# Kernel tuning notes

Hardware: AMD Instinct MI355X
Metric: run time of the kernel (lower is better)

Reference implementation:

```python
import jax, jax.numpy as jnp
import numpy as np


def conv1x1(x, w, b):
    # x: [B,C,H,W], w: [O,C], b: [O]
    return jnp.einsum('bchw,oc->bohw', x, w) + b[None, :, None, None]


def conv2d_same(x, w, b):
    # x: [B,C,H,W], w: [O,I,kh,kw]
    y = jax.lax.conv_general_dilated(x, w, (1, 1), 'SAME',
                                     dimension_numbers=('NCHW', 'OIHW', 'NCHW'))
    return y + b[None, :, None, None]


def l2norm_c(x):
    # F.normalize(x, dim=1): x / max(||x||_2, eps)
    n = jnp.sqrt(jnp.sum(x * x, axis=1, keepdims=True))
    return x / jnp.maximum(n, 1e-12)


def warp_volume(k, disps, directs):
    # Plane-sweep warp. grid_sample(bilinear, border, align_corners=True) with a
    # pure horizontal shift: y-coords equal the identity grid exactly, so
    # bilinear interpolation reduces to 1-D interpolation along W.
    # k: [B,C,H,W], disps: [D], directs: [B,1,1,1] -> [B,C,H,W,D]
    B, C, H, W = k.shape
    dt = k.dtype
    base = jnp.arange(W, dtype=dt)                                   # pixel x
    # normalized shift disp*2 maps to disp*(W-1) pixels (align_corners=True)
    shift = disps.astype(dt)[None, :, None] * directs.reshape(B, 1, 1) * (W - 1)
    px = jnp.clip(base[None, None, :] + shift, 0.0, W - 1)            # [B,D,W] (border pad)
    x0 = jnp.floor(px).astype(jnp.int32)
    x1 = jnp.minimum(x0 + 1, W - 1)
    f = (px - x0.astype(dt))[:, None, None, :, :]                     # [B,1,1,D,W]
    gather = jax.vmap(lambda xb, ib: xb[:, :, ib])                    # [B,C,H,D,W]
    g0 = gather(k, x0)
    g1 = gather(k, x1)
    wk = g0 * (1.0 - f) + g1 * f                                      # [B,C,H,D,W]
    return jnp.transpose(wk, (0, 1, 2, 4, 3))                         # [B,C,H,W,D]


def setup_inputs() -> dict:
    key = jax.random.key(0)
    ks = jax.random.split(key, 16)
    B, C, H, W = 4, 128, 96, 320
    Cm, D = C // 4, 32
    f32 = jnp.float32
    inp = {
        't_feat': jax.random.normal(ks[0], (B, C, H, W), f32),
        's_feat': jax.random.normal(ks[1], (B, C, H, W), f32),
        'directs': jnp.ones((B, 1, 1, 1), f32),
        'image_shape': 320,
        'disps': jnp.arange(D, dtype=f32) * 0.01,
        'wq': jax.random.normal(ks[2], (Cm, C), f32) * 0.05,
        'bq': jnp.zeros((Cm,), f32),
        'wkc': jax.random.normal(ks[3], (Cm, C), f32) * 0.05,
        'bkc': jnp.zeros((Cm,), f32),
        'metric': jnp.eye(Cm, dtype=f32),
        'alpha': jnp.asarray(10.0, f32),
        'beta': jnp.asarray(0.0, f32),
        'w_cf': jax.random.normal(ks[4], (1, 1, 3, 3), f32) * 0.1,
        'b_cf': jnp.zeros((1,), f32),
        'w_da': jax.random.normal(ks[5], (D, 2 * Cm), f32) * 0.05,
        'b_da': jnp.zeros((D,), f32),
        'w_ex': jax.random.normal(ks[6], (C, D), f32) * 0.05,
        'b_ex': jnp.zeros((C,), f32),
        'w_fg': jax.random.normal(ks[7], (1, 2 * C), f32) * 0.05,
        'b_fg': jnp.zeros((1,), f32),
        'w_rd': jax.random.normal(ks[8], (C, C, 3, 3), f32) * 0.02,
        'b_rd': jnp.zeros((C,), f32),
        'w_se1': jax.random.normal(ks[9], (C // 16, C), f32) * 0.1,
        'w_se2': jax.random.normal(ks[10], (C, C // 16), f32) * 0.1,
    }
    return inp


def reference(t_feat, s_feat, directs, image_shape, disps,
              wq, bq, wkc, bkc, metric, alpha, beta,
              w_cf, b_cf, w_da, b_da, w_ex, b_ex, w_fg, b_fg,
              w_rd, b_rd, w_se1, w_se2):
    del image_shape  # only used when train_image_size is set (it is None here)
    q = l2norm_c(conv1x1(t_feat, wq, bq))          # [B,Cm,H,W]
    k = l2norm_c(conv1x1(s_feat, wkc, bkc))        # [B,Cm,H,W]
    warped = warp_volume(k, disps, directs)        # [B,Cm,H,W,D]
    M = 0.5 * (metric + metric.T)
    q_proj = jnp.einsum('bchw,cd->bdhw', q, M)
    sim = jnp.einsum('bdhw,bdhwk->bhwk', q_proj, warped)
    sim = jnp.tanh(alpha * sim + beta)             # [B,H,W,D]
    Cv = jnp.transpose(sim, (0, 3, 1, 2))          # [B,D,H,W]
    B, D, H, W = Cv.shape
    # Conv3d(1,1,(1,3,3)) == per-slice 2D 3x3 conv
    Cf = conv2d_same(Cv.reshape(B * D, 1, H, W), w_cf, b_cf).reshape(B, D, H, W)
    k_mean = warped.mean(axis=-1)                  # [B,Cm,H,W]
    da = jax.nn.sigmoid(conv1x1(jnp.concatenate([q, k_mean], axis=1), w_da, b_da))
    Cf = Cf * da
    P = jax.nn.softmax(Cf, axis=1)                 # [B,D,H,W]
    cost_feat = conv1x1(P, w_ex, b_ex)             # [B,C,H,W]
    g = jax.nn.sigmoid(conv1x1(jnp.concatenate([t_feat, cost_feat], axis=1), w_fg, b_fg))
    fused = g * t_feat + (1.0 - g) * cost_feat
    x = conv2d_same(fused, w_rd, b_rd)
    # SELayer(reduction=16)
    y = x.mean(axis=(2, 3))                        # [B,C]
    y = jax.nn.relu(y @ w_se1.T)
    y = jax.nn.sigmoid(y @ w_se2.T)
    x = x * y[:, :, None, None]
    x = jax.nn.elu(x)
    return (x, P)
```

## Files before the change

### kernel.cpp

```cpp
#include <hip/hip_runtime.h>
#include <hip/hip_bf16.h>
#include <math.h>


typedef __hip_bfloat16 bf16;
typedef unsigned short u16;
typedef __attribute__((ext_vector_type(8))) __bf16 bf16x8;
typedef __attribute__((ext_vector_type(4))) float f4;

#define DEVI static __device__ __forceinline__
DEVI float bf2f(bf16 x) { return __bfloat162float(x); }
DEVI bf16  f2bf(float x) { return __float2bfloat16(x); }
DEVI u16 bfbits(float x) { bf16 h = f2bf(x); return *(u16*)&h; }
DEVI float sigmoidf_(float x) { return 1.0f / (1.0f + expf(-x)); }

constexpr int B_ = 4, C_ = 128, H_ = 96, W_ = 320, CM = 32, D_ = 32;
constexpr int HW = H_ * W_;
constexpr int QPLANE = CM * HW;
constexpr int XN = B_ * C_ * HW;
constexpr int PLN = B_ * D_ * HW;

__device__ __align__(16) float g_scratch[8 * PLN];
__device__ __align__(16) u16   g_fused[XN];
__device__ __align__(16) u16   g_wt[9 * 128 * 128];
__device__ float g_ysum[512];
__device__ float g_se[512];
__device__ int   g_flag[1];

DEVI float ldin(const void* p, int i, int isb) {
    float v;
    if (isb) v = bf2f(((const bf16*)p)[i]);
    else     v = ((const float*)p)[i];
    return v;
}
DEVI void stout(void* p, int i, float v, int isb) {
    if (isb) ((bf16*)p)[i] = f2bf(v);
    else     ((float*)p)[i] = v;
}

__global__ __launch_bounds__(256) void k_detect(
    const void* __restrict__ t, const void* __restrict__ wqp)
{
    __shared__ int bad;
    int tid = threadIdx.x;
    if (tid == 0) bad = 0;
    __syncthreads();
    int mybad = 0;
    for (int i = tid; i < 4096; i += 256) {
        float v = bf2f(((const bf16*)t)[i]);
        if (!(v == v) || fabsf(v) > 64.0f) mybad = 1;
        float u = bf2f(((const bf16*)wqp)[i]);
        if (!(u == u) || fabsf(u) > 64.0f) mybad = 1;
    }
    if (mybad) atomicOr(&bad, 1);
    g_ysum[tid] = 0.f;
    g_ysum[tid + 256] = 0.f;
    __syncthreads();
    if (tid == 0) g_flag[0] = bad ? 0 : 1;
}

__global__ __launch_bounds__(256) void k_wprep(
    const void* __restrict__ w_rd, u16* __restrict__ gw)
{
    int isb = g_flag[0];
    int i = blockIdx.x * 256 + threadIdx.x;
    if (i >= 9 * 128 * 128) return;
    int pos = i >> 14, rem = i & 16383, co = rem >> 7, ci = rem & 127;
    gw[i] = bfbits(ldin(w_rd, (co * 128 + ci) * 9 + pos, isb));
}

__global__ __launch_bounds__(320) void k_qk(
    const void* __restrict__ t_feat, const void* __restrict__ s_feat,
    const void* __restrict__ wq, const void* __restrict__ bq,
    const void* __restrict__ wkc, const void* __restrict__ bkc,
    float* __restrict__ qout, float* __restrict__ kout)
{
    __shared__ float WST[C_ * CM];
    __shared__ float BS[CM];
    int isb = g_flag[0];
    int h = blockIdx.x, b = blockIdx.y, which = blockIdx.z;
    const void* in = which ? s_feat : t_feat;
    const void* wm = which ? wkc : wq;
    const void* bb = which ? bkc : bq;
    float* out = which ? kout : qout;
    int tid = threadIdx.x;
    for (int i = tid; i < C_ * CM; i += 320) {
        int o = i >> 7, c = i & 127;
        WST[c * CM + o] = ldin(wm, i, isb);
    }
    if (tid < CM) BS[tid] = ldin(bb, tid, isb);
    __syncthreads();
    int w = tid;
    float acc[CM];
    #pragma unroll
    for (int o = 0; o < CM; o++) acc[o] = BS[o];
    int base = (b * C_) * HW + h * W_ + w;
    for (int c = 0; c < C_; c++) {
        float v = ldin(in, base + c * HW, isb);
        #pragma unroll
        for (int o = 0; o < CM; o++) acc[o] += v * WST[c * CM + o];
    }
    float n = 0.f;
    #pragma unroll
    for (int o = 0; o < CM; o++) n += acc[o] * acc[o];
    float s = 1.0f / fmaxf(sqrtf(n), 1e-12f);
    float* op = out + (b * CM) * HW + h * W_ + w;
    #pragma unroll
    for (int o = 0; o < CM; o++) op[o * HW] = acc[o] * s;
}

__global__ __launch_bounds__(320, 3) void k_cost(
    const float* __restrict__ qbuf, const float* __restrict__ kbuf,
    const void* __restrict__ metric, const void* __restrict__ disps,
    const void* __restrict__ directs, const void* __restrict__ alpha_p,
    const void* __restrict__ beta_p, const void* __restrict__ w_da,
    const void* __restrict__ b_da,
    float* __restrict__ Cv, float* __restrict__ da)
{
    __shared__ float KS[CM][W_];
    __shared__ float MS[CM][CM];
    __shared__ float WDA[D_ * 64];
    __shared__ float BDA[D_];
    __shared__ float SH[D_];
    int isb = g_flag[0];
    int h = blockIdx.x, b = blockIdx.y, tid = threadIdx.x, w = tid;
    for (int i = tid; i < CM * CM; i += 320) {
        int c = i >> 5, d = i & 31;
        MS[c][d] = 0.5f * (ldin(metric, c * CM + d, isb) + ldin(metric, d * CM + c, isb));
    }
    for (int i = tid; i < D_ * 64; i += 320) WDA[i] = ldin(w_da, i, isb);
    if (tid < D_) {
        BDA[tid] = ldin(b_da, tid, isb);
        SH[tid] = ldin(disps, tid, isb) * ldin(directs, b, isb) * (float)(W_ - 1);
    }
    const float* kp = kbuf + b * QPLANE + h * W_;
    for (int c = 0; c < CM; c++) KS[c][w] = kp[c * HW + w];
    __syncthreads();

    float qp[CM], dqa[CM];
    #pragma unroll
    for (int d = 0; d < CM; d++) { qp[d] = 0.f; dqa[d] = 0.f; }
    const float* qpp = qbuf + b * QPLANE + h * W_ + w;
    for (int c = 0; c < CM; c++) {
        float v = qpp[c * HW];
        #pragma unroll
        for (int d = 0; d < CM; d++) qp[d] += v * MS[c][d];
        #pragma unroll
        for (int d = 0; d < D_; d++) dqa[d] += v * WDA[d * 64 + c];
    }

    float km[CM];
    #pragma unroll
    for (int c = 0; c < CM; c++) km[c] = 0.f;
    float alpha = ldin(alpha_p, 0, isb), beta = ldin(beta_p, 0, isb);
    float* cvp = Cv + (b * D_) * HW + h * W_ + w;
    for (int d = 0; d < D_; d++) {
        float px = fminf(fmaxf((float)w + SH[d], 0.f), (float)(W_ - 1));
        int x0 = (int)floorf(px);
        int x1 = min(x0 + 1, W_ - 1);
        float f = px - (float)x0;
        float sim = 0.f;
        #pragma unroll
        for (int c = 0; c < CM; c++) {
            float g0 = KS[c][x0], g1 = KS[c][x1];
            float val = g0 * (1.0f - f) + g1 * f;
            sim += qp[c] * val;
            km[c] += val;
        }
        cvp[d * HW] = tanhf(alpha * sim + beta);
    }

    #pragma unroll
    for (int c = 0; c < CM; c++) km[c] *= (1.0f / (float)D_);
    float* dap = da + (b * D_) * HW + h * W_ + w;
    for (int d = 0; d < D_; d++) {
        float s = BDA[d] + dqa[d];
        #pragma unroll
        for (int c = 0; c < CM; c++) s += WDA[d * 64 + 32 + c] * km[c];
        dap[d * HW] = sigmoidf_(s);
    }
}

__global__ __launch_bounds__(320) void k_cf_softmax(
    const float* __restrict__ Cv, const float* __restrict__ da,
    const void* __restrict__ w_cf, const void* __restrict__ b_cf,
    float* __restrict__ Pf, void* __restrict__ dout)
{
    __shared__ float R[3][322];
    int isb = g_flag[0];
    int h = blockIdx.x, b = blockIdx.y, tid = threadIdx.x, w = tid;
    float wcf[9];
    #pragma unroll
    for (int i = 0; i < 9; i++) wcf[i] = ldin(w_cf, i, isb);
    float bcf = ldin(b_cf, 0, isb);
    float vals[D_];
    for (int d = 0; d < D_; d++) {
        const float* base = Cv + ((b * D_ + d) * H_) * W_;
        #pragma unroll
        for (int r = 0; r < 3; r++) {
            int hh = h + r - 1;
            R[r][w + 1] = (hh >= 0 && hh < H_) ? base[hh * W_ + w] : 0.f;
        }
        if (tid == 0) {
            R[0][0] = R[1][0] = R[2][0] = 0.f;
            R[0][321] = R[1][321] = R[2][321] = 0.f;
        }
        __syncthreads();
        float s = bcf;
        #pragma unroll
        for (int r = 0; r < 3; r++)
            #pragma unroll
            for (int kw = 0; kw < 3; kw++)
                s += R[r][w + kw] * wcf[r * 3 + kw];
        vals[d] = s * da[((b * D_ + d) * H_ + h) * W_ + w];
        __syncthreads();
    }
    float m = vals[0];
    #pragma unroll
    for (int d = 1; d < D_; d++) m = fmaxf(m, vals[d]);
    float sum = 0.f;
    #pragma unroll
    for (int d = 0; d < D_; d++) { vals[d] = expf(vals[d] - m); sum += vals[d]; }
    float inv = 1.0f / sum;
    int o = (b * D_) * HW + h * W_ + w;
    #pragma unroll
    for (int d = 0; d < D_; d++) {
        float p = vals[d] * inv;
        Pf[o + d * HW] = p;
        stout(dout, XN + o + d * HW, p, isb);
    }
}

__global__ __launch_bounds__(320) void k_fuse(
    const float* __restrict__ Pf, const void* __restrict__ t_feat,
    const void* __restrict__ w_ex, const void* __restrict__ b_ex,
    const void* __restrict__ w_fg, const void* __restrict__ b_fg,
    u16* __restrict__ gf)
{
    __shared__ float WEX[C_ * D_];
    __shared__ float BEX[C_];
    __shared__ float WFG[2 * C_];
    int isb = g_flag[0];
    int h = blockIdx.x, b = blockIdx.y, tid = threadIdx.x, w = tid;
    for (int i = tid; i < C_ * D_; i += 320) WEX[i] = ldin(w_ex, i, isb);
    if (tid < C_) BEX[tid] = ldin(b_ex, tid, isb);
    for (int i = tid; i < 2 * C_; i += 320) WFG[i] = ldin(w_fg, i, isb);
    __syncthreads();
    float p[D_];
    const float* pp = Pf + (b * D_) * HW + h * W_ + w;
    #pragma unroll
    for (int d = 0; d < D_; d++) p[d] = pp[d * HW];
    int tbase = (b * C_) * HW + h * W_ + w;
    float gacc = ldin(b_fg, 0, isb);
    for (int c = 0; c < C_; c++) {
        float cost = BEX[c];
        #pragma unroll
        for (int d = 0; d < D_; d++) cost += WEX[c * D_ + d] * p[d];
        float tv = ldin(t_feat, tbase + c * HW, isb);
        gacc += WFG[c] * tv + WFG[C_ + c] * cost;
    }
    float g = sigmoidf_(gacc);
    unsigned int* gfo = (unsigned int*)gf + ((b * H_ + h) * W_ + w) * 64;
    for (int c = 0; c < C_; c += 2) {
        float c0 = BEX[c], c1 = BEX[c + 1];
        #pragma unroll
        for (int d = 0; d < D_; d++) {
            c0 += WEX[c * D_ + d] * p[d];
            c1 += WEX[(c + 1) * D_ + d] * p[d];
        }
        float t0 = ldin(t_feat, tbase + c * HW, isb);
        float t1 = ldin(t_feat, tbase + (c + 1) * HW, isb);
        float v0 = g * t0 + (1.0f - g) * c0;
        float v1 = g * t1 + (1.0f - g) * c1;
        gfo[c >> 1] = ((unsigned int)bfbits(v1) << 16) | bfbits(v0);
    }
}

__global__ __launch_bounds__(128, 2) void k_conv3(
    const u16* __restrict__ gf, const u16* __restrict__ gw,
    const void* __restrict__ b_rd, float* __restrict__ xf)
{
    __shared__ u16 IN[6 * 34 * 40];
    __shared__ u16 WS[128 * 40];
    int isb = g_flag[0];
    int tid = threadIdx.x;
    int wave = tid >> 6, lane = tid & 63;
    int l15 = lane & 15, kq = lane >> 4;
    int w0 = blockIdx.x * 32, h0 = blockIdx.y * 4, b = blockIdx.z;

    f4 acc[4][8];
    #pragma unroll
    for (int mt = 0; mt < 4; mt++)
        #pragma unroll
        for (int nt = 0; nt < 8; nt++) acc[mt][nt] = (f4){0.f, 0.f, 0.f, 0.f};

    float bias[8];
    #pragma unroll
    for (int nt = 0; nt < 8; nt++) bias[nt] = ldin(b_rd, nt * 16 + l15, isb);

    for (int cb = 0; cb < 128; cb += 32) {
        __syncthreads();
        for (int s = tid; s < 204 * 4; s += 128) {
            int p = s >> 2, q = s & 3;
            int hp = p / 34, wp = p - hp * 34;
            int hg = h0 - 1 + hp, wg = w0 - 1 + wp;
            uint4 v = make_uint4(0u, 0u, 0u, 0u);
            if (hg >= 0 && hg < H_ && wg >= 0 && wg < W_)
                v = *(const uint4*)(gf + ((((b * H_ + hg) * W_ + wg) << 7) + cb + q * 8));
            *(uint4*)(&IN[(hp * 34 + wp) * 40 + q * 8]) = v;
        }
        for (int pos = 0; pos < 9; pos++) {
            __syncthreads();
            for (int s = tid; s < 128 * 4; s += 128) {
                int co = s >> 2, q = s & 3;
                *(uint4*)(&WS[co * 40 + q * 8]) =
                    *(const uint4*)(gw + (((pos * 128 + co) << 7) + cb + q * 8));
            }
            __syncthreads();
            int kh = pos / 3, kw = pos - kh * 3;
            bf16x8 bfr[8];
            #pragma unroll
            for (int nt = 0; nt < 8; nt++)
                bfr[nt] = *(bf16x8*)(&WS[(nt * 16 + l15) * 40 + kq * 8]);
            #pragma unroll
            for (int mt = 0; mt < 4; mt++) {
                int px = wave * 64 + mt * 16 + l15;
                int row = (px >> 5) + kh, col = (px & 31) + kw;
                bf16x8 afr = *(bf16x8*)(&IN[(row * 34 + col) * 40 + kq * 8]);
                #pragma unroll
                for (int nt = 0; nt < 8; nt++)
                    acc[mt][nt] = __builtin_amdgcn_mfma_f32_16x16x32_bf16(
                        afr, bfr[nt], acc[mt][nt], 0, 0, 0);
            }
        }
    }
    #pragma unroll
    for (int nt = 0; nt < 8; nt++) {
        int co = nt * 16 + l15;
        float ps = 0.f;
        #pragma unroll
        for (int mt = 0; mt < 4; mt++) {
            #pragma unroll
            for (int r = 0; r < 4; r++) {
                int px = wave * 64 + mt * 16 + kq * 4 + r;
                float v = acc[mt][nt][r] + bias[nt];
                ps += v;
                xf[((b * C_ + co) * H_ + h0 + (px >> 5)) * W_ + w0 + (px & 31)] = v;
            }
        }
        ps += __shfl_xor(ps, 16);
        ps += __shfl_xor(ps, 32);
        if (lane < 16) atomicAdd(&g_ysum[b * C_ + co], ps);
    }
}

__global__ __launch_bounds__(512) void k_se(
    const void* __restrict__ w_se1, const void* __restrict__ w_se2)
{
    __shared__ float YM[B_ * C_];
    __shared__ float Y1[B_ * 8];
    int isb = g_flag[0];
    int tid = threadIdx.x;
    YM[tid] = g_ysum[tid] * (1.0f / (float)HW);
    __syncthreads();
    if (tid < 32) {
        int b = tid >> 3, j = tid & 7;
        float s = 0.f;
        for (int c = 0; c < C_; c++) s += YM[b * C_ + c] * ldin(w_se1, j * C_ + c, isb);
        Y1[tid] = fmaxf(s, 0.f);
    }
    __syncthreads();
    int b = tid >> 7, c = tid & 127;
    float s = 0.f;
    #pragma unroll
    for (int j = 0; j < 8; j++) s += Y1[b * 8 + j] * ldin(w_se2, c * 8 + j, isb);
    g_se[tid] = sigmoidf_(s);
}

__global__ __launch_bounds__(256) void k_elu(
    const float* __restrict__ xf, void* __restrict__ dout)
{
    int isb = g_flag[0];
    int idx = blockIdx.x * 256 + threadIdx.x;
    if (idx >= XN) return;
    int plane = idx / HW;
    float v = xf[idx] * g_se[plane];
    stout(dout, idx, v > 0.f ? v : expm1f(v), isb);
}

extern "C" void kernel_launch(void* const* d_in, const int* in_sizes, int n_in,
                              void* d_out, int out_size, void* d_ws, size_t ws_size,
                              hipStream_t stream)
{
    const void* t_feat  = d_in[0];
    const void* s_feat  = d_in[1];
    const void* directs = d_in[2];
    const void* disps   = d_in[4];
    const void* wq      = d_in[5];
    const void* bq      = d_in[6];
    const void* wkc     = d_in[7];
    const void* bkc     = d_in[8];
    const void* metric  = d_in[9];
    const void* alpha   = d_in[10];
    const void* beta    = d_in[11];
    const void* w_cf    = d_in[12];
    const void* b_cf    = d_in[13];
    const void* w_da    = d_in[14];
    const void* b_da    = d_in[15];
    const void* w_ex    = d_in[16];
    const void* b_ex    = d_in[17];
    const void* w_fg    = d_in[18];
    const void* b_fg    = d_in[19];
    const void* w_rd    = d_in[20];
    const void* b_rd    = d_in[21];
    const void* w_se1   = d_in[22];
    const void* w_se2   = d_in[23];
    (void)in_sizes; (void)n_in; (void)out_size; (void)d_ws; (void)ws_size;

    float* base = nullptr;
    (void)hipGetSymbolAddress((void**)&base, HIP_SYMBOL(g_scratch));
    u16* gf = nullptr;
    (void)hipGetSymbolAddress((void**)&gf, HIP_SYMBOL(g_fused));
    u16* gw = nullptr;
    (void)hipGetSymbolAddress((void**)&gw, HIP_SYMBOL(g_wt));
    float* qb = base;
    float* kb = base + PLN;
    float* Cv = base + 2 * PLN;
    float* da = base + 3 * PLN;
    float* Pf = base + 4 * PLN;
    float* xf = base + 4 * PLN;

    k_detect<<<1, 256, 0, stream>>>(t_feat, wq);
    k_wprep<<<576, 256, 0, stream>>>(w_rd, gw);
    k_qk<<<dim3(H_, B_, 2), 320, 0, stream>>>(t_feat, s_feat, wq, bq, wkc, bkc, qb, kb);
    k_cost<<<dim3(H_, B_), 320, 0, stream>>>(qb, kb, metric, disps, directs,
                                             alpha, beta, w_da, b_da, Cv, da);
    k_cf_softmax<<<dim3(H_, B_), 320, 0, stream>>>(Cv, da, w_cf, b_cf, Pf, d_out);
    k_fuse<<<dim3(H_, B_), 320, 0, stream>>>(Pf, t_feat, w_ex, b_ex, w_fg, b_fg, gf);
    k_conv3<<<dim3(10, 24, 4), 128, 0, stream>>>(gf, gw, b_rd, xf);
    k_se<<<1, 512, 0, stream>>>(w_se1, w_se2);
    k_elu<<<(XN + 255) / 256, 256, 0, stream>>>(xf, d_out);
}
```

Measured before the change: 661.6 us.

## Double-buffer conv3 weight tiles, split output channels across 4 waves, swizzle LDS

The 3x3 conv kernel now runs 4 waves per block instead of 2, with each wave computing half of the output channels for half of the pixels. The per-position weight tile is double-buffered: the next slice is prefetched into registers during the MFMA loop, then written to the alternate LDS buffer, so one barrier per step replaces two. LDS addresses are XOR-swizzled to reduce bank conflicts. The cost is more LDS per block and a higher occupancy target in the launch bounds, which may cause register pressure.

```diff
diff --git a/kernel.cpp b/kernel.cpp
--- a/kernel.cpp
+++ b/kernel.cpp
@@ -276,73 +276,96 @@
     }
 }
 
-__global__ __launch_bounds__(128, 2) void k_conv3(
+__global__ __launch_bounds__(256, 4) void k_conv3(
     const u16* __restrict__ gf, const u16* __restrict__ gw,
     const void* __restrict__ b_rd, float* __restrict__ xf)
 {
-    __shared__ u16 IN[6 * 34 * 40];
-    __shared__ u16 WS[128 * 40];
+    __shared__ u16 IN[204 * 40];
+    __shared__ u16 WS[2][128 * 40];
     int isb = g_flag[0];
     int tid = threadIdx.x;
     int wave = tid >> 6, lane = tid & 63;
+    int wr = wave >> 1, wc = wave & 1;
     int l15 = lane & 15, kq = lane >> 4;
     int w0 = blockIdx.x * 32, h0 = blockIdx.y * 4, b = blockIdx.z;
 
-    f4 acc[4][8];
+    f4 acc[4][4];
     #pragma unroll
     for (int mt = 0; mt < 4; mt++)
         #pragma unroll
-        for (int nt = 0; nt < 8; nt++) acc[mt][nt] = (f4){0.f, 0.f, 0.f, 0.f};
-
-    float bias[8];
-    #pragma unroll
-    for (int nt = 0; nt < 8; nt++) bias[nt] = ldin(b_rd, nt * 16 + l15, isb);
-
+        for (int nt = 0; nt < 4; nt++) acc[mt][nt] = (f4){0.f, 0.f, 0.f, 0.f};
+
+    float bias[4];
+    #pragma unroll
+    for (int nt = 0; nt < 4; nt++) bias[nt] = ldin(b_rd, wc * 64 + nt * 16 + l15, isb);
+
+    #pragma unroll
+    for (int i = 0; i < 2; i++) {
+        int s = tid + i * 256, co = s >> 2, q = s & 3;
+        *(uint4*)(&WS[0][co * 40 + ((q * 8) ^ (co & 8))]) =
+            *(const uint4*)(gw + ((co << 7) + q * 8));
+    }
+
+    int step = 0;
     for (int cb = 0; cb < 128; cb += 32) {
         __syncthreads();
-        for (int s = tid; s < 204 * 4; s += 128) {
+        for (int s = tid; s < 204 * 4; s += 256) {
             int p = s >> 2, q = s & 3;
             int hp = p / 34, wp = p - hp * 34;
             int hg = h0 - 1 + hp, wg = w0 - 1 + wp;
             uint4 v = make_uint4(0u, 0u, 0u, 0u);
             if (hg >= 0 && hg < H_ && wg >= 0 && wg < W_)
                 v = *(const uint4*)(gf + ((((b * H_ + hg) * W_ + wg) << 7) + cb + q * 8));
-            *(uint4*)(&IN[(hp * 34 + wp) * 40 + q * 8]) = v;
-        }
-        for (int pos = 0; pos < 9; pos++) {
-            __syncthreads();
-            for (int s = tid; s < 128 * 4; s += 128) {
-                int co = s >> 2, q = s & 3;
-                *(uint4*)(&WS[co * 40 + q * 8]) =
-                    *(const uint4*)(gw + (((pos * 128 + co) << 7) + cb + q * 8));
+            *(uint4*)(&IN[p * 40 + ((q * 8) ^ (p & 8))]) = v;
+        }
+        __syncthreads();
+        for (int pos = 0; pos < 9; pos++, step++) {
+            int cur = step & 1;
+            uint4 wreg0, wreg1;
+            int have = (step < 35);
+            int pn = (pos == 8) ? 0 : pos + 1;
+            int cbn = (pos == 8) ? cb + 32 : cb;
+            if (have) {
+                int co0 = tid >> 2, q0 = tid & 3;
+                wreg0 = *(const uint4*)(gw + (((pn * 128 + co0) << 7) + cbn + q0 * 8));
+                int s1 = tid + 256, co1 = s1 >> 2, q1 = s1 & 3;
+                wreg1 = *(const uint4*)(gw + (((pn * 128 + co1) << 7) + cbn + q1 * 8));
             }
-            __syncthreads();
             int kh = pos / 3, kw = pos - kh * 3;
-            bf16x8 bfr[8];
+            bf16x8 bfr[4];
             #pragma unroll
-            for (int nt = 0; nt < 8; nt++)
-                bfr[nt] = *(bf16x8*)(&WS[(nt * 16 + l15) * 40 + kq * 8]);
+            for (int nt = 0; nt < 4; nt++) {
+                int co = wc * 64 + nt * 16 + l15;
+                bfr[nt] = *(bf16x8*)(&WS[cur][co * 40 + ((kq * 8) ^ (co & 8))]);
+            }
             #pragma unroll
             for (int mt = 0; mt < 4; mt++) {
-                int px = wave * 64 + mt * 16 + l15;
-                int row = (px >> 5) + kh, col = (px & 31) + kw;
-                bf16x8 afr = *(bf16x8*)(&IN[(row * 34 + col) * 40 + kq * 8]);
+                int px = wr * 64 + mt * 16 + l15;
+                int rc = ((px >> 5) + kh) * 34 + (px & 31) + kw;
+                bf16x8 afr = *(bf16x8*)(&IN[rc * 40 + ((kq * 8) ^ (rc & 8))]);
                 #pragma unroll
-                for (int nt = 0; nt < 8; nt++)
+                for (int nt = 0; nt < 4; nt++)
                     acc[mt][nt] = __builtin_amdgcn_mfma_f32_16x16x32_bf16(
                         afr, bfr[nt], acc[mt][nt], 0, 0, 0);
             }
-        }
-    }
-    #pragma unroll
-    for (int nt = 0; nt < 8; nt++) {
-        int co = nt * 16 + l15;
+            if (have) {
+                int co0 = tid >> 2, q0 = tid & 3;
+                *(uint4*)(&WS[cur ^ 1][co0 * 40 + ((q0 * 8) ^ (co0 & 8))]) = wreg0;
+                int s1 = tid + 256, co1 = s1 >> 2, q1 = s1 & 3;
+                *(uint4*)(&WS[cur ^ 1][co1 * 40 + ((q1 * 8) ^ (co1 & 8))]) = wreg1;
+            }
+            __syncthreads();
+        }
+    }
+    #pragma unroll
+    for (int nt = 0; nt < 4; nt++) {
+        int co = wc * 64 + nt * 16 + l15;
         float ps = 0.f;
         #pragma unroll
         for (int mt = 0; mt < 4; mt++) {
             #pragma unroll
             for (int r = 0; r < 4; r++) {
-                int px = wave * 64 + mt * 16 + kq * 4 + r;
+                int px = wr * 64 + mt * 16 + kq * 4 + r;
                 float v = acc[mt][nt][r] + bias[nt];
                 ps += v;
                 xf[((b * C_ + co) * H_ + h0 + (px >> 5)) * W_ + w0 + (px & 31)] = v;
@@ -437,7 +460,7 @@
                                              alpha, beta, w_da, b_da, Cv, da);
     k_cf_softmax<<<dim3(H_, B_), 320, 0, stream>>>(Cv, da, w_cf, b_cf, Pf, d_out);
     k_fuse<<<dim3(H_, B_), 320, 0, stream>>>(Pf, t_feat, w_ex, b_ex, w_fg, b_fg, gf);
-    k_conv3<<<dim3(10, 24, 4), 128, 0, stream>>>(gf, gw, b_rd, xf);
+    k_conv3<<<dim3(10, 24, 4), 256, 0, stream>>>(gf, gw, b_rd, xf);
     k_se<<<1, 512, 0, stream>>>(w_se1, w_se2);
     k_elu<<<(XN + 255) / 256, 256, 0, stream>>>(xf, d_out);
 }
```

New measurement: 698.5 us. 1.06x slower.
